# Kernel tuning notes

Measured on AMD Instinct MI355X. Metric: run time of the kernel, lower is better.

Reference implementation:

```python
import jax, jax.numpy as jnp
import numpy as np

N, E, D, EF, C, G, NPG = 50000, 500000, 16, 8, 10, 500, 100
NUM_LAYERS = 3
EPS = 1e-5


def setup_inputs() -> dict:
    key = jax.random.key(0)
    ks = jax.random.split(key, 16)
    s = 0.1
    return {
        'x': jax.random.normal(ks[0], (N, D), jnp.float32),
        'edge_attr': jax.random.normal(ks[1], (E, EF), jnp.float32),
        # edge MLP (shared across all NNConv layers, as in the source)
        'edge_w1': jax.random.normal(ks[2], (EF, D), jnp.float32) * s,
        'edge_b1': jnp.zeros((D,), jnp.float32),
        'edge_w2': jax.random.normal(ks[3], (D, D * D), jnp.float32) * s,
        'edge_b2': jnp.zeros((D * D,), jnp.float32),
        # per-layer NNConv root weight + bias
        'root': jax.random.normal(ks[4], (NUM_LAYERS, D, D), jnp.float32) * s,
        'conv_bias': jnp.zeros((NUM_LAYERS, D), jnp.float32),
        # per-layer BatchNorm affine params
        'bn_gamma': jnp.ones((NUM_LAYERS, D), jnp.float32),
        'bn_beta': jnp.zeros((NUM_LAYERS, D), jnp.float32),
        # readout MLP
        'fc1_w': jax.random.normal(ks[5], (4 * D, D), jnp.float32) * s,
        'fc1_b': jnp.zeros((D,), jnp.float32),
        'fc2_w': jax.random.normal(ks[6], (D, C), jnp.float32) * s,
        'fc2_b': jnp.zeros((C,), jnp.float32),
        # graph structure (constants w.r.t. grads)
        'edge_index': jax.random.randint(ks[7], (2, E), 0, N, dtype=jnp.int32),
        'lengths': jnp.full((G,), NPG, dtype=jnp.int32),
    }


def reference(x, edge_attr, edge_w1, edge_b1, edge_w2, edge_b2, root,
              conv_bias, bn_gamma, bn_beta, fc1_w, fc1_b, fc2_w, fc2_b,
              edge_index, lengths):
    src, dst = edge_index[0], edge_index[1]
    # Edge MLP -> per-edge weight matrices [E, D, D] (edge_attr is layer-invariant,
    # so the shared edge_model output is computed once).
    h_e = jnp.tanh(edge_attr @ edge_w1 + edge_b1)
    W = (h_e @ edge_w2 + edge_b2).reshape(E, D, D)
    # in-degree for mean aggregation (nodes with no incoming edges -> 0)
    deg = jax.ops.segment_sum(jnp.ones((E,), x.dtype), dst, num_segments=N)
    deg = jnp.maximum(deg, 1.0)[:, None]

    h = x
    for l in range(NUM_LAYERS):
        # NNConv: gather -> per-edge matvec -> scatter-mean, plus root term + bias
        msg = jnp.einsum('ei,eio->eo', h[src], W)          # [E, D]
        agg = jax.ops.segment_sum(msg, dst, num_segments=N) / deg
        h = agg + h @ root[l] + conv_bias[l]
        # BatchNorm over nodes (training-mode batch statistics, biased var)
        mu = h.mean(axis=0)
        var = h.var(axis=0)
        h = (h - mu) * jax.lax.rsqrt(var + EPS) * bn_gamma[l] + bn_beta[l]
        h = jnp.tanh(h)  # Dropout is identity in eval mode

    hidden = h
    # ragged segment pooling: graph id per node from lengths
    seg = jnp.repeat(jnp.arange(G), lengths, total_repeat_length=N)
    sum_p = jax.ops.segment_sum(hidden, seg, num_segments=G)
    cnt = jnp.maximum(lengths.astype(hidden.dtype), 1)[:, None]
    mean_p = sum_p / cnt
    max_p = jax.ops.segment_max(hidden, seg, num_segments=G)
    min_p = jax.ops.segment_min(hidden, seg, num_segments=G)
    pooled = jnp.concatenate([mean_p, max_p, min_p, sum_p], axis=1)  # [G, 4D]

    fc = jnp.tanh(pooled @ fc1_w + fc1_b)
    fc = fc @ fc2_w + fc2_b
    out = jax.nn.log_softmax(fc, axis=1)
    return hidden, pooled, fc, out
```

## Files before the change

### kernel.cpp

```cpp
#include <hip/hip_runtime.h>

#define D 16
#define EFD 8
#define NREP 64
#define TSTRIDE 272

typedef unsigned short u16;
typedef unsigned int u32;

__device__ __forceinline__ u16 f2bf(float x) {
    u32 u = __float_as_uint(x);
    u += 0x7fffu + ((u >> 16) & 1u);
    return (u16)(u >> 16);
}
__device__ __forceinline__ void unpack8(uint4 u, float* f) {
    f[0] = __uint_as_float(u.x << 16); f[1] = __uint_as_float(u.x & 0xffff0000u);
    f[2] = __uint_as_float(u.y << 16); f[3] = __uint_as_float(u.y & 0xffff0000u);
    f[4] = __uint_as_float(u.z << 16); f[5] = __uint_as_float(u.z & 0xffff0000u);
    f[6] = __uint_as_float(u.w << 16); f[7] = __uint_as_float(u.w & 0xffff0000u);
}


__global__ void k_zero2(int* a, int na, float* b, int nb) {
    int i = blockIdx.x * 256 + threadIdx.x;
    if (i < na) a[i] = 0;
    if (i < nb) b[i] = 0.f;
}


__global__ void k_rank2(const int* __restrict__ src, const int* __restrict__ dst,
                        int* __restrict__ cntS, int* __restrict__ cntD,
                        int* __restrict__ rankS, int* __restrict__ rankD, int E_) {
    int e = blockIdx.x * 256 + threadIdx.x;
    if (e < E_) {
        rankS[e] = atomicAdd(&cntS[src[e]], 1);
        rankD[e] = atomicAdd(&cntD[dst[e]], 1);
    }
}


__global__ void k_scanA2(const int* __restrict__ cnt2, int* __restrict__ offs2,
                         int* __restrict__ bsum2, int n, int nScan) {
    __shared__ int s[1024];
    int half = blockIdx.x / nScan;
    int blk  = blockIdx.x % nScan;
    const int* c = cnt2 + (size_t)half * n;
    int* of = offs2 + (size_t)half * (n + 1);
    int* bs = bsum2 + half * 64;
    int i = blk * 1024 + threadIdx.x;
    int v = (i < n) ? c[i] : 0;
    s[threadIdx.x] = v;
    __syncthreads();
    for (int d = 1; d < 1024; d <<= 1) {
        int t = (threadIdx.x >= d) ? s[threadIdx.x - d] : 0;
        __syncthreads();
        s[threadIdx.x] += t;
        __syncthreads();
    }
    int incl = s[threadIdx.x];
    if (i < n) of[i] = incl - v;
    if (threadIdx.x == 1023) bs[blk] = incl;
}

__global__ void k_scanC2(int* __restrict__ offs2, const int* __restrict__ bsum2,
                         int n, int nScan, int total) {
    __shared__ int s[64];
    int half = blockIdx.x / nScan;
    int blk  = blockIdx.x % nScan;
    int* of = offs2 + (size_t)half * (n + 1);
    const int* bs = bsum2 + half * 64;
    if (threadIdx.x < 64) s[threadIdx.x] = (threadIdx.x < nScan) ? bs[threadIdx.x] : 0;
    __syncthreads();
    if (threadIdx.x < 64) {
        for (int d = 1; d < 64; d <<= 1) {
            int t = (threadIdx.x >= d) ? s[threadIdx.x - d] : 0;
            __syncthreads();
            s[threadIdx.x] += t;
            __syncthreads();
        }
    } else {
        for (int d = 1; d < 64; d <<= 1) { __syncthreads(); __syncthreads(); }
    }
    int base = (blk == 0) ? 0 : s[blk - 1];
    int i = blk * 1024 + threadIdx.x;
    if (i < n) of[i] += base;
    else if (i == n) of[n] = total;
}


__global__ void k_place_he(const int* __restrict__ src, const int* __restrict__ dst,
                           const int* __restrict__ rankS, const int* __restrict__ rankD,
                           const int* __restrict__ offsS, const int* __restrict__ offsD,
                           const float* __restrict__ ea, const float* __restrict__ w1,
                           const float* __restrict__ b1,
                           u16* __restrict__ hE, int* __restrict__ permInv, int E_) {
    __shared__ float w1s[EFD * D];
    __shared__ float b1s[D];
    if (threadIdx.x < EFD * D) w1s[threadIdx.x] = w1[threadIdx.x];
    if (threadIdx.x < D) b1s[threadIdx.x] = b1[threadIdx.x];
    __syncthreads();
    int e = blockIdx.x * 256 + threadIdx.x;
    if (e >= E_) return;
    int p = offsS[src[e]] + rankS[e];
    int q = offsD[dst[e]] + rankD[e];
    permInv[p] = q;
    const float4* a4 = (const float4*)(ea + (size_t)e * EFD);
    float4 x0 = a4[0], x1 = a4[1];
    u32 pk[8];
#pragma unroll
    for (int v = 0; v < 8; v++) {
        float o0, o1;
#pragma unroll
        for (int h = 0; h < 2; h++) {
            int o = 2 * v + h;
            float u0 = x0.x * w1s[0 * D + o] + x0.y * w1s[1 * D + o]
                     + x0.z * w1s[2 * D + o] + x0.w * w1s[3 * D + o];
            float u1 = x1.x * w1s[4 * D + o] + x1.y * w1s[5 * D + o]
                     + x1.z * w1s[6 * D + o] + x1.w * w1s[7 * D + o];
            float t = tanhf(b1s[o] + u0 + u1);
            if (h == 0) o0 = t; else o1 = t;
        }
        pk[v] = (u32)f2bf(o0) | ((u32)f2bf(o1) << 16);
    }
    uint4* h8 = (uint4*)(hE + (size_t)p * D);
    h8[0] = make_uint4(pk[0], pk[1], pk[2], pk[3]);
    h8[1] = make_uint4(pk[4], pk[5], pk[6], pk[7]);
}


__global__ void k_Tmsg(const float* __restrict__ hin, const float* __restrict__ statsPrev,
                       const float* __restrict__ gamma, const float* __restrict__ beta,
                       float* __restrict__ hout, const float* __restrict__ w2,
                       const float* __restrict__ b2, const u16* __restrict__ hE,
                       const int* __restrict__ offsS, const int* __restrict__ permInv,
                       u16* __restrict__ msg, int n, int useBN) {
    __shared__ float hs[16 * D];
    __shared__ float Tt[16 * TSTRIDE];
    __shared__ float sstats[32];
    int tid = threadIdx.x;
    int j = tid >> 4, o = tid & 15;
    int base = blockIdx.x * 16;
    int node = base + j;
    float fn = (float)n;
    int p0 = 0, p1 = 0;
    if (node < n) { p0 = offsS[node]; p1 = offsS[node + 1]; }
    int qPre = 0;
    uint4 a0, a1;
    if (p0 < p1) {
        qPre = permInv[p0];
        const uint4* he8 = (const uint4*)(hE + (size_t)p0 * D);
        a0 = he8[0]; a1 = he8[1];
    }
    float w16[16], b16[16];
#pragma unroll
    for (int i = 0; i < 16; i++) w16[i] = w2[j * 256 + i * 16 + o];
#pragma unroll
    for (int i = 0; i < 16; i++) b16[i] = b2[i * 16 + o];
    if (useBN && tid < 32) {
        float a = 0.f;
#pragma unroll 8
        for (int r = 0; r < NREP; r++) a += statsPrev[r * 32 + tid];
        sstats[tid] = a;
    }
    __syncthreads();
    {
        float hv = 0.f;
        if (node < n) {
            float xin = hin[(size_t)node * D + o];
            if (useBN) {
                float mu = sstats[o] / fn;
                float var = sstats[16 + o] / fn - mu * mu;
                hv = tanhf((xin - mu) * rsqrtf(var + 1e-5f) * gamma[o] + beta[o]);
                hout[(size_t)node * D + o] = hv;
            } else {
                hv = xin;
            }
        }
        hs[tid] = hv;
    }
    __syncthreads();
    {
        const float4* hs4 = (const float4*)hs;
#pragma unroll
        for (int nb = 0; nb < 16; nb++) {
            float4 h0 = hs4[nb * 4 + 0], h1 = hs4[nb * 4 + 1];
            float4 h2 = hs4[nb * 4 + 2], h3 = hs4[nb * 4 + 3];
            float q0 = h0.x * w16[0]  + h0.y * w16[1]  + h0.z * w16[2]  + h0.w * w16[3];
            float q1 = h1.x * w16[4]  + h1.y * w16[5]  + h1.z * w16[6]  + h1.w * w16[7];
            float q2 = h2.x * w16[8]  + h2.y * w16[9]  + h2.z * w16[10] + h2.w * w16[11];
            float q3 = h3.x * w16[12] + h3.y * w16[13] + h3.z * w16[14] + h3.w * w16[15];
            Tt[nb * TSTRIDE + tid] = (q0 + q1) + (q2 + q3);
        }
        float4 h0 = hs4[j * 4 + 0], h1 = hs4[j * 4 + 1];
        float4 h2 = hs4[j * 4 + 2], h3 = hs4[j * 4 + 3];
        float q0 = h0.x * b16[0]  + h0.y * b16[1]  + h0.z * b16[2]  + h0.w * b16[3];
        float q1 = h1.x * b16[4]  + h1.y * b16[5]  + h1.z * b16[6]  + h1.w * b16[7];
        float q2 = h2.x * b16[8]  + h2.y * b16[9]  + h2.z * b16[10] + h2.w * b16[11];
        float q3 = h3.x * b16[12] + h3.y * b16[13] + h3.z * b16[14] + h3.w * b16[15];
        Tt[j * TSTRIDE + 256 + o] = (q0 + q1) + (q2 + q3);
    }
    __syncthreads();
    if (node < n) {
        float tr[16];
#pragma unroll
        for (int j2 = 0; j2 < 16; j2++) tr[j2] = Tt[j * TSTRIDE + j2 * 16 + o];
        float tb = Tt[j * TSTRIDE + 256 + o];
        int q = qPre;
        for (int p = p0; p < p1; p++) {
            uint4 c0 = a0, c1 = a1;
            int qc = q;
            if (p + 1 < p1) {
                q = permInv[p + 1];
                const uint4* n8 = (const uint4*)(hE + (size_t)(p + 1) * D);
                a0 = n8[0]; a1 = n8[1];
            }
            float e[16];
            unpack8(c0, e); unpack8(c1, e + 8);
            float s0 = e[0]  * tr[0]  + e[1]  * tr[1]  + e[2]  * tr[2]  + e[3]  * tr[3];
            float s1 = e[4]  * tr[4]  + e[5]  * tr[5]  + e[6]  * tr[6]  + e[7]  * tr[7];
            float s2 = e[8]  * tr[8]  + e[9]  * tr[9]  + e[10] * tr[10] + e[11] * tr[11];
            float s3 = e[12] * tr[12] + e[13] * tr[13] + e[14] * tr[14] + e[15] * tr[15];
            msg[(size_t)qc * D + o] = f2bf(tb + ((s0 + s1) + (s2 + s3)));
        }
    }
}


__global__ void k_agg(const float* __restrict__ h, const u16* __restrict__ msg,
                      const int* __restrict__ offsD, const float* __restrict__ root_l,
                      const float* __restrict__ cbias, float* __restrict__ hpre,
                      float* __restrict__ statsR, int n) {
    __shared__ float rootS[D * D];
    __shared__ float red[256], red2[256];
    if (threadIdx.x < D * D) rootS[threadIdx.x] = root_l[threadIdx.x];
    __syncthreads();
    int slot = threadIdx.x >> 4, o = threadIdx.x & 15;
    int node = blockIdx.x * 16 + slot;
    float acc = 0.f;
    if (node < n) {
        int p0 = offsD[node], p1 = offsD[node + 1];
        float sum = 0.f;
        int p = p0;
        for (; p + 4 <= p1; p += 4) {
            float a0 = __uint_as_float((u32)msg[(size_t)(p + 0) * D + o] << 16);
            float a1 = __uint_as_float((u32)msg[(size_t)(p + 1) * D + o] << 16);
            float a2 = __uint_as_float((u32)msg[(size_t)(p + 2) * D + o] << 16);
            float a3 = __uint_as_float((u32)msg[(size_t)(p + 3) * D + o] << 16);
            sum += (a0 + a1) + (a2 + a3);
        }
        for (; p < p1; p++) sum += __uint_as_float((u32)msg[(size_t)p * D + o] << 16);
        float deg = (float)((p1 - p0) > 1 ? (p1 - p0) : 1);
        const float* hr = h + (size_t)node * D;
        float r0 = hr[0]  * rootS[0 * D + o]  + hr[1]  * rootS[1 * D + o]
                 + hr[2]  * rootS[2 * D + o]  + hr[3]  * rootS[3 * D + o];
        float r1 = hr[4]  * rootS[4 * D + o]  + hr[5]  * rootS[5 * D + o]
                 + hr[6]  * rootS[6 * D + o]  + hr[7]  * rootS[7 * D + o];
        float r2 = hr[8]  * rootS[8 * D + o]  + hr[9]  * rootS[9 * D + o]
                 + hr[10] * rootS[10 * D + o] + hr[11] * rootS[11 * D + o];
        float r3 = hr[12] * rootS[12 * D + o] + hr[13] * rootS[13 * D + o]
                 + hr[14] * rootS[14 * D + o] + hr[15] * rootS[15 * D + o];
        acc = sum / deg + cbias[o] + ((r0 + r1) + (r2 + r3));
        hpre[(size_t)node * D + o] = acc;
    }
    red[threadIdx.x] = acc;
    red2[threadIdx.x] = acc * acc;
    __syncthreads();
    for (int off = 128; off >= 16; off >>= 1) {
        if (threadIdx.x < off) {
            red[threadIdx.x] += red[threadIdx.x + off];
            red2[threadIdx.x] += red2[threadIdx.x + off];
        }
        __syncthreads();
    }
    if (threadIdx.x < 32) {
        float v = (threadIdx.x < 16) ? red[threadIdx.x] : red2[threadIdx.x - 16];
        atomicAdd(&statsR[(blockIdx.x & (NREP - 1)) * 32 + threadIdx.x], v);
    }
}


__global__ void k_readout(const float* __restrict__ hpre, const float* __restrict__ statsR,
                          const float* __restrict__ gamma, const float* __restrict__ beta,
                          const int* __restrict__ lengths,
                          const float* __restrict__ w1, const float* __restrict__ b1,
                          const float* __restrict__ w2, const float* __restrict__ b2,
                          float* __restrict__ outHidden, float* __restrict__ outPooled,
                          float* __restrict__ fcOut, float* __restrict__ lsmOut,
                          int Gc, int n) {
    __shared__ int sl[512];
    __shared__ float sstats[32];
    int tid = threadIdx.x;
    int g = blockIdx.x;
    if (tid < 32) {
        float a = 0.f;
#pragma unroll 8
        for (int r = 0; r < NREP; r++) a += statsR[r * 32 + tid];
        sstats[tid] = a;
    }
    int v = (tid < Gc) ? lengths[tid] : 0;
    sl[tid] = v;
    __syncthreads();
    for (int d = 1; d < 512; d <<= 1) {
        int t = (tid >= d) ? sl[tid - d] : 0;
        __syncthreads();
        sl[tid] += t;
        __syncthreads();
    }
    int n1 = sl[g];
    int n0 = n1 - lengths[g];
    float fn = (float)n;
    int slot = tid >> 4, o = tid & 15;
    float mu = sstats[o] / fn;
    float var = sstats[16 + o] / fn - mu * mu;
    float rstd = rsqrtf(var + 1e-5f);
    float gm = gamma[o], bt = beta[o];
    float s = 0.f, mx = -3.402823466e38f, mn = 3.402823466e38f;
    for (int nd = n0 + slot; nd < n1; nd += 32) {
        float xin = hpre[(size_t)nd * D + o];
        float x = tanhf((xin - mu) * rstd * gm + bt);
        outHidden[(size_t)nd * D + o] = x;
        s += x;
        mx = fmaxf(mx, x);
        mn = fminf(mn, x);
    }
    __shared__ float rs[512], rmx[512], rmn[512];
    rs[tid] = s; rmx[tid] = mx; rmn[tid] = mn;
    __syncthreads();
    for (int off = 256; off >= 16; off >>= 1) {
        if (tid < off) {
            rs[tid] += rs[tid + off];
            rmx[tid] = fmaxf(rmx[tid], rmx[tid + off]);
            rmn[tid] = fminf(rmn[tid], rmn[tid + off]);
        }
        __syncthreads();
    }
    __shared__ float p64[64], t16[16], f10[10];
    __shared__ float mred, lred;
    if (tid < 16) {
        float cnt = fmaxf((float)(n1 - n0), 1.f);
        float sum = rs[tid];
        float* row = outPooled + (size_t)g * 64;
        float mean = sum / cnt;
        p64[tid] = mean;          row[tid] = mean;
        p64[16 + tid] = rmx[tid]; row[16 + tid] = rmx[tid];
        p64[32 + tid] = rmn[tid]; row[32 + tid] = rmn[tid];
        p64[48 + tid] = sum;      row[48 + tid] = sum;
    }
    __syncthreads();
    if (tid < 16) {
        float a = b1[tid];
        for (int k = 0; k < 64; k++) a += p64[k] * w1[k * 16 + tid];
        t16[tid] = tanhf(a);
    }
    __syncthreads();
    if (tid < 10) {
        float a = b2[tid];
        for (int oo = 0; oo < 16; oo++) a += t16[oo] * w2[oo * 10 + tid];
        f10[tid] = a;
        fcOut[(size_t)g * 10 + tid] = a;
    }
    __syncthreads();
    if (tid == 0) {
        float m = f10[0];
        for (int c = 1; c < 10; c++) m = fmaxf(m, f10[c]);
        float se = 0.f;
        for (int c = 0; c < 10; c++) se += expf(f10[c] - m);
        mred = m;
        lred = logf(se);
    }
    __syncthreads();
    if (tid < 10)
        lsmOut[(size_t)g * 10 + tid] = f10[tid] - mred - lred;
}


extern "C" void kernel_launch(void* const* d_in, const int* in_sizes, int n_in,
                              void* d_out, int out_size, void* d_ws, size_t ws_size,
                              hipStream_t stream) {
    const float* x    = (const float*)d_in[0];
    const float* ea   = (const float*)d_in[1];
    const float* ew1  = (const float*)d_in[2];
    const float* eb1  = (const float*)d_in[3];
    const float* ew2  = (const float*)d_in[4];
    const float* eb2  = (const float*)d_in[5];
    const float* root = (const float*)d_in[6];
    const float* cb   = (const float*)d_in[7];
    const float* gam  = (const float*)d_in[8];
    const float* bet  = (const float*)d_in[9];
    const float* f1w  = (const float*)d_in[10];
    const float* f1b  = (const float*)d_in[11];
    const float* f2w  = (const float*)d_in[12];
    const float* f2b  = (const float*)d_in[13];
    const int* eidx   = (const int*)d_in[14];
    const int* lens   = (const int*)d_in[15];

    int N  = in_sizes[0] / D;
    int E_ = in_sizes[1] / EFD;
    int Gc = in_sizes[15];
    const int* srcIdx = eidx;
    const int* dstIdx = eidx + E_;

    float* outHidden = (float*)d_out;
    float* outPooled = outHidden + (size_t)N * D;
    float* outFc     = outPooled + (size_t)Gc * 4 * D;
    float* outLsm    = outFc + (size_t)Gc * 10;

    char* wsp = (char*)d_ws;
    size_t off = 0;
    auto alloc = [&](size_t bytes) -> void* {
        void* p = wsp + off;
        off = (off + bytes + 255) & ~(size_t)255;
        return p;
    };
    int*   cnt2    = (int*)alloc((size_t)2 * N * 4);
    int*   offs2   = (int*)alloc((size_t)2 * (N + 1) * 4);
    int*   bsum2   = (int*)alloc(128 * 4);
    int*   rankS   = (int*)alloc((size_t)E_ * 4);
    int*   rankD   = (int*)alloc((size_t)E_ * 4);
    int*   permInv = (int*)alloc((size_t)E_ * 4);
    u16*   hE      = (u16*)alloc((size_t)E_ * D * 2);
    u16*   msg     = (u16*)alloc((size_t)E_ * D * 2);
    float* bufA    = (float*)alloc((size_t)N * D * 4);
    float* tmp     = (float*)alloc((size_t)N * D * 4);
    float* statsR3 = (float*)alloc((size_t)3 * NREP * 32 * 4);

    int* offsS = offs2;
    int* offsD = offs2 + (N + 1);
    int nScan = (N + 1023) / 1024;

    k_zero2<<<(2 * N + 255) / 256, 256, 0, stream>>>(cnt2, 2 * N, statsR3, 3 * NREP * 32);
    k_rank2<<<(E_ + 255) / 256, 256, 0, stream>>>(srcIdx, dstIdx, cnt2, cnt2 + N,
                                                  rankS, rankD, E_);
    k_scanA2<<<2 * nScan, 1024, 0, stream>>>(cnt2, offs2, bsum2, N, nScan);
    k_scanC2<<<2 * nScan, 1024, 0, stream>>>(offs2, bsum2, N, nScan, E_);
    k_place_he<<<(E_ + 255) / 256, 256, 0, stream>>>(srcIdx, dstIdx, rankS, rankD,
                                                     offsS, offsD, ea, ew1, eb1,
                                                     hE, permInv, E_);

    for (int l = 0; l < 3; l++) {
        const float* hin   = (l == 0) ? x : tmp;
        const float* hroot = (l == 0) ? x : bufA;
        float* statsCur = statsR3 + (size_t)l * NREP * 32;
        const float* statsPrev = statsR3 + (size_t)(l - 1) * NREP * 32;
        k_Tmsg<<<(N + 15) / 16, 256, 0, stream>>>(
            hin, (l == 0) ? nullptr : statsPrev,
            (l == 0) ? nullptr : gam + (size_t)(l - 1) * 16,
            (l == 0) ? nullptr : bet + (size_t)(l - 1) * 16,
            bufA, ew2, eb2, hE, offsS, permInv, msg, N, (l == 0) ? 0 : 1);
        k_agg<<<(N + 15) / 16, 256, 0, stream>>>(hroot, msg, offsD,
                                                 root + (size_t)l * 256, cb + (size_t)l * 16,
                                                 tmp, statsCur, N);
    }

    k_readout<<<Gc, 512, 0, stream>>>(tmp, statsR3 + (size_t)2 * NREP * 32,
                                      gam + 32, bet + 32, lens, f1w, f1b, f2w, f2b,
                                      outHidden, outPooled, outFc, outLsm, Gc, N);
}
```

Baseline: 291.5 us.

## Stage per-edge hidden vectors cooperatively through shared memory in chunks of eight

In the message kernel, the 16 lanes of each node now load eight edges' packed bf16 hidden vectors together (one uint4 per lane) plus permutation indices. They double-buffer these chunks in shared memory and broadcast indices with shuffles, replacing the previous pattern where every lane redundantly loaded the same 32-byte row each edge. The aggregation kernel's gather loop is also unrolled from 4 to 8 messages per iteration. This cuts redundant global loads and exposes more memory parallelism, at the cost of extra shared memory, wave-level shuffles, and reliance on lockstep execution within a wavefront with no explicit barrier between buffer writes and reads.

Result: no change. 287.2 us (-1.5%).

```diff
diff --git a/kernel.cpp b/kernel.cpp
--- a/kernel.cpp
+++ b/kernel.cpp
@@ -128,6 +128,8 @@
 }
 
 
+#define SBSTRIDE 17
+
 __global__ void k_Tmsg(const float* __restrict__ hin, const float* __restrict__ statsPrev,
                        const float* __restrict__ gamma, const float* __restrict__ beta,
                        float* __restrict__ hout, const float* __restrict__ w2,
@@ -137,20 +139,32 @@
     __shared__ float hs[16 * D];
     __shared__ float Tt[16 * TSTRIDE];
     __shared__ float sstats[32];
+    __shared__ uint4 sbuf[4 * 2 * 4 * SBSTRIDE + 4];
     int tid = threadIdx.x;
     int j = tid >> 4, o = tid & 15;
+    int w = tid >> 6, jj = j & 3;
     int base = blockIdx.x * 16;
     int node = base + j;
     float fn = (float)n;
     int p0 = 0, p1 = 0;
     if (node < n) { p0 = offsS[node]; p1 = offsS[node + 1]; }
-    int qPre = 0;
-    uint4 a0, a1;
-    if (p0 < p1) {
-        qPre = permInv[p0];
-        const uint4* he8 = (const uint4*)(hE + (size_t)p0 * D);
-        a0 = he8[0]; a1 = he8[1];
-    }
+    int deg = p1 - p0;
+    int nCh = (deg + 7) >> 3;
+    uint4* buf0 = &sbuf[((w * 2 + 0) * 4 + jj) * SBSTRIDE];
+    uint4* buf1 = &sbuf[((w * 2 + 1) * 4 + jj) * SBSTRIDE];
+
+    uint4 regH = make_uint4(0, 0, 0, 0);
+    int regQ = 0;
+    if (deg > 0) {
+        int pr = p0 + (o >> 1);
+        int pc = (pr < p1) ? pr : p1 - 1;
+        regH = ((const uint4*)(hE + (size_t)pc * D))[o & 1];
+        if (o < 8) {
+            int pq = p0 + o;
+            regQ = permInv[(pq < p1) ? pq : p1 - 1];
+        }
+    }
+
     float w16[16], b16[16];
 #pragma unroll
     for (int i = 0; i < 16; i++) w16[i] = w2[j * 256 + i * 16 + o];
@@ -200,27 +214,42 @@
         Tt[j * TSTRIDE + 256 + o] = (q0 + q1) + (q2 + q3);
     }
     __syncthreads();
-    if (node < n) {
+    if (node < n && deg > 0) {
         float tr[16];
 #pragma unroll
         for (int j2 = 0; j2 < 16; j2++) tr[j2] = Tt[j * TSTRIDE + j2 * 16 + o];
         float tb = Tt[j * TSTRIDE + 256 + o];
-        int q = qPre;
-        for (int p = p0; p < p1; p++) {
-            uint4 c0 = a0, c1 = a1;
-            int qc = q;
-            if (p + 1 < p1) {
-                q = permInv[p + 1];
-                const uint4* n8 = (const uint4*)(hE + (size_t)(p + 1) * D);
-                a0 = n8[0]; a1 = n8[1];
+        buf0[o] = regH;
+        for (int c = 0; c < nCh; c++) {
+            uint4* cur = (c & 1) ? buf1 : buf0;
+            uint4* nxt = (c & 1) ? buf0 : buf1;
+            uint4 nH; int nQ = 0;
+            if (c + 1 < nCh) {
+                int pr = p0 + (c + 1) * 8 + (o >> 1);
+                int pc = (pr < p1) ? pr : p1 - 1;
+                nH = ((const uint4*)(hE + (size_t)pc * D))[o & 1];
+                if (o < 8) {
+                    int pq = p0 + (c + 1) * 8 + o;
+                    nQ = permInv[(pq < p1) ? pq : p1 - 1];
+                }
             }
-            float e[16];
-            unpack8(c0, e); unpack8(c1, e + 8);
-            float s0 = e[0]  * tr[0]  + e[1]  * tr[1]  + e[2]  * tr[2]  + e[3]  * tr[3];
-            float s1 = e[4]  * tr[4]  + e[5]  * tr[5]  + e[6]  * tr[6]  + e[7]  * tr[7];
-            float s2 = e[8]  * tr[8]  + e[9]  * tr[9]  + e[10] * tr[10] + e[11] * tr[11];
-            float s3 = e[12] * tr[12] + e[13] * tr[13] + e[14] * tr[14] + e[15] * tr[15];
-            msg[(size_t)qc * D + o] = f2bf(tb + ((s0 + s1) + (s2 + s3)));
+            int eMax = deg - c * 8;
+            if (eMax > 8) eMax = 8;
+            for (int i = 0; i < eMax; i++) {
+                uint4 r0 = cur[2 * i], r1 = cur[2 * i + 1];
+                int qe = __shfl(regQ, jj * 16 + i);
+                float e[16];
+                unpack8(r0, e); unpack8(r1, e + 8);
+                float s0 = e[0]  * tr[0]  + e[1]  * tr[1]  + e[2]  * tr[2]  + e[3]  * tr[3];
+                float s1 = e[4]  * tr[4]  + e[5]  * tr[5]  + e[6]  * tr[6]  + e[7]  * tr[7];
+                float s2 = e[8]  * tr[8]  + e[9]  * tr[9]  + e[10] * tr[10] + e[11] * tr[11];
+                float s3 = e[12] * tr[12] + e[13] * tr[13] + e[14] * tr[14] + e[15] * tr[15];
+                msg[(size_t)qe * D + o] = f2bf(tb + ((s0 + s1) + (s2 + s3)));
+            }
+            if (c + 1 < nCh) {
+                nxt[o] = nH;
+                regQ = nQ;
+            }
         }
     }
 }
@@ -241,12 +270,16 @@
         int p0 = offsD[node], p1 = offsD[node + 1];
         float sum = 0.f;
         int p = p0;
-        for (; p + 4 <= p1; p += 4) {
+        for (; p + 8 <= p1; p += 8) {
             float a0 = __uint_as_float((u32)msg[(size_t)(p + 0) * D + o] << 16);
             float a1 = __uint_as_float((u32)msg[(size_t)(p + 1) * D + o] << 16);
             float a2 = __uint_as_float((u32)msg[(size_t)(p + 2) * D + o] << 16);
             float a3 = __uint_as_float((u32)msg[(size_t)(p + 3) * D + o] << 16);
-            sum += (a0 + a1) + (a2 + a3);
+            float a4 = __uint_as_float((u32)msg[(size_t)(p + 4) * D + o] << 16);
+            float a5 = __uint_as_float((u32)msg[(size_t)(p + 5) * D + o] << 16);
+            float a6 = __uint_as_float((u32)msg[(size_t)(p + 6) * D + o] << 16);
+            float a7 = __uint_as_float((u32)msg[(size_t)(p + 7) * D + o] << 16);
+            sum += ((a0 + a1) + (a2 + a3)) + ((a4 + a5) + (a6 + a7));
         }
         for (; p < p1; p++) sum += __uint_as_float((u32)msg[(size_t)p * D + o] << 16);
         float deg = (float)((p1 - p0) > 1 ? (p1 - p0) : 1);
```
